# Kernel tuning notes

Hardware: AMD Instinct MI355X
Metric: run time of the kernel (lower is better)

The kernel has to match this reference:

```python
import jax, jax.numpy as jnp
import numpy as np

T, B, F = 512, 256, 256
H1, H2, OUT = 128, 64, 5


def _gru_layer(x, w_ih, w_hh, b_ih, b_hh):
    """PyTorch-convention GRU over time-major x [T, B, F_in] -> [T, B, H].
    Gate order in weights: r, z, n. n = tanh(Wn x + bn_i + r * (Un h + bn_h))."""
    H = w_hh.shape[1]
    # Precompute input projections for all timesteps: [T, B, 3H]
    xp = jnp.einsum('tbf,gf->tbg', x, w_ih) + b_ih

    def step(h, xp_t):
        hp = h @ w_hh.T + b_hh  # [B, 3H]
        xr, xz, xn = jnp.split(xp_t, 3, axis=-1)
        hr, hz, hn = jnp.split(hp, 3, axis=-1)
        r = jax.nn.sigmoid(xr + hr)
        z = jax.nn.sigmoid(xz + hz)
        n = jnp.tanh(xn + r * hn)
        h_new = (1.0 - z) * n + z * h
        return h_new, h_new

    h0 = jnp.zeros((x.shape[1], H), dtype=x.dtype)
    _, ys = jax.lax.scan(step, h0, xp)
    return ys  # [T, B, H]


def setup_inputs() -> dict:
    key = jax.random.key(0)
    ks = jax.random.split(key, 12)
    s1 = 1.0 / np.sqrt(H1)
    s2 = 1.0 / np.sqrt(H2)
    return {
        'x': jax.random.normal(ks[0], (T, B, F), dtype=jnp.float32),
        'w_ih1': jax.random.uniform(ks[1], (3 * H1, F), jnp.float32, -s1, s1),
        'w_hh1': jax.random.uniform(ks[2], (3 * H1, H1), jnp.float32, -s1, s1),
        'b_ih1': jax.random.uniform(ks[3], (3 * H1,), jnp.float32, -s1, s1),
        'b_hh1': jax.random.uniform(ks[4], (3 * H1,), jnp.float32, -s1, s1),
        'w_ih2': jax.random.uniform(ks[5], (3 * H2, H1), jnp.float32, -s2, s2),
        'w_hh2': jax.random.uniform(ks[6], (3 * H2, H2), jnp.float32, -s2, s2),
        'b_ih2': jax.random.uniform(ks[7], (3 * H2,), jnp.float32, -s2, s2),
        'b_hh2': jax.random.uniform(ks[8], (3 * H2,), jnp.float32, -s2, s2),
        'lin_w': jax.random.uniform(ks[9], (OUT, H2), jnp.float32, -s2, s2),
        'lin_b': jax.random.uniform(ks[10], (OUT,), jnp.float32, -s2, s2),
    }


def reference(x, w_ih1, w_hh1, b_ih1, b_hh1, w_ih2, w_hh2, b_ih2, b_hh2, lin_w, lin_b):
    h1 = _gru_layer(x, w_ih1, w_hh1, b_ih1, b_hh1)   # [T, B, 128]
    h2 = _gru_layer(h1, w_ih2, w_hh2, b_ih2, b_hh2)  # [T, B, 64]
    # Faithful to the original: x[:, -1, :] selects the last BATCH element
    # across all timesteps (time-major layout), giving [T, 64].
    last = h2[:, -1, :]
    return last @ lin_w.T + lin_b  # [T, 5]
```

## Files before the change

### kernel.cpp

```cpp
#include <hip/hip_runtime.h>
#include <hip/hip_bf16.h>

#define T_STEPS 512
#define BATCH   256
#define FDIM    256
#define H1      128
#define H2      64
#define OUT_N   5
#define CAT     (H1 + H2)
#define LOG2E   1.4426950408889634f

#if __has_builtin(__builtin_amdgcn_exp2f)
#define EXP2F(x) __builtin_amdgcn_exp2f(x)
#else
#define EXP2F(x) exp2f(x)
#endif
#if __has_builtin(__builtin_amdgcn_rcpf)
#define RCPF(x) __builtin_amdgcn_rcpf(x)
#else
#define RCPF(x) (1.0f / (x))
#endif

template<int CTRL>
__device__ __forceinline__ float dpp_add(float v) {
    int s = __builtin_amdgcn_update_dpp(0, __float_as_int(v), CTRL, 0xF, 0xF, true);
    return v + __int_as_float(s);
}
__device__ __forceinline__ float sig_scaled(float a) {
    return RCPF(1.0f + EXP2F(a));
}
__device__ __forceinline__ float tanh_scaled(float a) {
    return fmaf(-2.0f, RCPF(EXP2F(a) + 1.0f), 1.0f);
}

__global__ __launch_bounds__(256) void xp1_kernel(
    const float* __restrict__ x,
    const float* __restrict__ w_ih1,
    const float* __restrict__ b_ih1,
    const float* __restrict__ b_hh1,
    float* __restrict__ xp)
{
    __shared__ float xrow[FDIM];
    const int t = blockIdx.x;
    const float* xr = x + (size_t)t * BATCH * FDIM + (size_t)(BATCH - 1) * FDIM;
    if (threadIdx.x < FDIM / 4) {
        ((float4*)xrow)[threadIdx.x] = ((const float4*)xr)[threadIdx.x];
    }
    __syncthreads();
    const int q = threadIdx.x >> 2;
    const int s = threadIdx.x & 3;
    #pragma unroll
    for (int pass = 0; pass < 6; ++pass) {
        const int g = pass * 64 + q;
        const float* w = w_ih1 + (size_t)g * FDIM + (s << 2);
        float acc = 0.0f;
        #pragma unroll
        for (int c = 0; c < 16; ++c) {
            float4 wv = *(const float4*)(w + 16 * c);
            const float* xv = xrow + (s << 2) + 16 * c;
            acc = fmaf(wv.x, xv[0], acc);
            acc = fmaf(wv.y, xv[1], acc);
            acc = fmaf(wv.z, xv[2], acc);
            acc = fmaf(wv.w, xv[3], acc);
        }
        acc = dpp_add<0xB1>(acc);
        acc = dpp_add<0x4E>(acc);
        if (s == 0) {
            const bool isN = (g >= 2 * H1);
            const float badd  = isN ? 0.0f : b_hh1[g];
            const float scale = isN ? (2.0f * LOG2E) : (-LOG2E);
            xp[t * (3 * H1) + g] = scale * (acc + b_ih1[g] + badd);
        }
    }
}

__global__ __launch_bounds__(1024) void gru_seq_kernel(
    const float* __restrict__ xp,
    const float* __restrict__ w_hh1, const float* __restrict__ b_hh1,
    const float* __restrict__ w_ih2, const float* __restrict__ b_ih2,
    const float* __restrict__ w_hh2, const float* __restrict__ b_hh2,
    float* __restrict__ h2_all)
{
    const int tid = threadIdx.x;
    __shared__ float cat0[CAT];
    __shared__ float cat1[CAT];
    if (tid < CAT) { cat0[tid] = 0.0f; cat1[tid] = 0.0f; }

    const float sRZ = -LOG2E, sN = 2.0f * LOG2E;

    if (tid < 512) {
        const int j1 = tid >> 2, s1 = tid & 3;
        float w1r[32], w1z[32], w1n[32];
        {
            const float* br = w_hh1 + (size_t)(         j1) * H1;
            const float* bz = w_hh1 + (size_t)(H1     + j1) * H1;
            const float* bn = w_hh1 + (size_t)(2 * H1 + j1) * H1;
            #pragma unroll
            for (int c = 0; c < 8; c++) {
                const int kk = (s1 << 2) + 16 * c;
                float4 vr = *(const float4*)(br + kk);
                float4 vz = *(const float4*)(bz + kk);
                float4 vn = *(const float4*)(bn + kk);
                w1r[4*c+0]=sRZ*vr.x; w1r[4*c+1]=sRZ*vr.y; w1r[4*c+2]=sRZ*vr.z; w1r[4*c+3]=sRZ*vr.w;
                w1z[4*c+0]=sRZ*vz.x; w1z[4*c+1]=sRZ*vz.y; w1z[4*c+2]=sRZ*vz.z; w1z[4*c+3]=sRZ*vz.w;
                w1n[4*c+0]=sN *vn.x; w1n[4*c+1]=sN *vn.y; w1n[4*c+2]=sN *vn.z; w1n[4*c+3]=sN *vn.w;
            }
        }
        const float bh1n_s = sN * b_hh1[2 * H1 + j1];
        const float* xq = xp + j1;
        float cxr = xq[0], cxz = xq[H1], cxn = xq[2 * H1];
        xq += 3 * H1;
        __syncthreads();

        {
            float nr = xq[0], nz = xq[H1], nn = xq[2 * H1]; xq += 3 * H1;
            const float r1 = sig_scaled(cxr);
            const float z1 = sig_scaled(cxz);
            const float n1 = tanh_scaled(fmaf(r1, bh1n_s, cxn));
            if (s1 == 0) cat0[j1] = (1.0f - z1) * n1;
            cxr = nr; cxz = nz; cxn = nn;
            __syncthreads();
        }

        #define L1_STEP(RP, WP, PREF) do {                                              \
            const float* hp = RP + (s1 << 2);                                           \
            float ar = 0.f, az = 0.f, an = 0.f;                                         \
            _Pragma("unroll")                                                           \
            for (int c = 0; c < 8; c++) {                                               \
                float4 h4 = *(const float4*)(hp + 16 * c);                              \
                ar=fmaf(w1r[4*c+0],h4.x,ar); az=fmaf(w1z[4*c+0],h4.x,az); an=fmaf(w1n[4*c+0],h4.x,an); \
                ar=fmaf(w1r[4*c+1],h4.y,ar); az=fmaf(w1z[4*c+1],h4.y,az); an=fmaf(w1n[4*c+1],h4.y,an); \
                ar=fmaf(w1r[4*c+2],h4.z,ar); az=fmaf(w1z[4*c+2],h4.z,az); an=fmaf(w1n[4*c+2],h4.z,an); \
                ar=fmaf(w1r[4*c+3],h4.w,ar); az=fmaf(w1z[4*c+3],h4.w,az); an=fmaf(w1n[4*c+3],h4.w,an); \
            }                                                                           \
            const float h1old = RP[j1];                                                 \
            float nr = 0.f, nz = 0.f, nn = 0.f;                                         \
            if (PREF) { nr = xq[0]; nz = xq[H1]; nn = xq[2 * H1]; xq += 3 * H1; }       \
            ar = dpp_add<0xB1>(ar); ar = dpp_add<0x4E>(ar);                             \
            az = dpp_add<0xB1>(az); az = dpp_add<0x4E>(az);                             \
            an = dpp_add<0xB1>(an); an = dpp_add<0x4E>(an);                             \
            const float r1 = sig_scaled(cxr + ar);                                      \
            const float z1 = sig_scaled(cxz + az);                                      \
            const float n1 = tanh_scaled(fmaf(r1, an + bh1n_s, cxn));                   \
            if (s1 == 0) WP[j1] = fmaf(z1, h1old - n1, n1);                             \
            cxr = nr; cxz = nz; cxn = nn;                                               \
        } while (0)

        #pragma unroll 1
        for (int i = 0; i < 255; i++) {
            L1_STEP(cat0, cat1, true);
            __syncthreads();
            L1_STEP(cat1, cat0, true);
            __syncthreads();
        }
        L1_STEP(cat0, cat1, false);
        __syncthreads();
        __syncthreads();
        #undef L1_STEP
    } else {
        const int t2 = tid - 512;
        const int j2 = t2 >> 3, s2 = t2 & 7;
        float w2r[24], w2z[24], w2n[24];
        {
            const float* ir  = w_ih2 + (size_t)(         j2) * H1;
            const float* iz  = w_ih2 + (size_t)(H2     + j2) * H1;
            const float* inn = w_ih2 + (size_t)(2 * H2 + j2) * H1;
            #pragma unroll
            for (int c = 0; c < 4; c++) {
                const int kk = (s2 << 2) + 32 * c;
                float4 vr = *(const float4*)(ir  + kk);
                float4 vz = *(const float4*)(iz  + kk);
                float4 vn = *(const float4*)(inn + kk);
                w2r[4*c+0]=sRZ*vr.x; w2r[4*c+1]=sRZ*vr.y; w2r[4*c+2]=sRZ*vr.z; w2r[4*c+3]=sRZ*vr.w;
                w2z[4*c+0]=sRZ*vz.x; w2z[4*c+1]=sRZ*vz.y; w2z[4*c+2]=sRZ*vz.z; w2z[4*c+3]=sRZ*vz.w;
                w2n[4*c+0]=sN *vn.x; w2n[4*c+1]=sN *vn.y; w2n[4*c+2]=sN *vn.z; w2n[4*c+3]=sN *vn.w;
            }
            const float* hr = w_hh2 + (size_t)(         j2) * H2;
            const float* hz = w_hh2 + (size_t)(H2     + j2) * H2;
            const float* hn = w_hh2 + (size_t)(2 * H2 + j2) * H2;
            #pragma unroll
            for (int c = 0; c < 2; c++) {
                const int kk = (s2 << 2) + 32 * c;
                const int o = 4 * (c + 4);
                float4 vr = *(const float4*)(hr + kk);
                float4 vz = *(const float4*)(hz + kk);
                float4 vn = *(const float4*)(hn + kk);
                w2r[o+0]=sRZ*vr.x; w2r[o+1]=sRZ*vr.y; w2r[o+2]=sRZ*vr.z; w2r[o+3]=sRZ*vr.w;
                w2z[o+0]=sRZ*vz.x; w2z[o+1]=sRZ*vz.y; w2z[o+2]=sRZ*vz.z; w2z[o+3]=sRZ*vz.w;
                w2n[o+0]=sN *vn.x; w2n[o+1]=sN *vn.y; w2n[o+2]=sN *vn.z; w2n[o+3]=sN *vn.w;
            }
        }
        const float b2r_s  = sRZ * (b_ih2[j2]      + b_hh2[j2]);
        const float b2z_s  = sRZ * (b_ih2[H2 + j2] + b_hh2[H2 + j2]);
        const float b2xn_s = sN  *  b_ih2[2 * H2 + j2];
        const float b2hn_s = sN  *  b_hh2[2 * H2 + j2];
        float* hout = h2_all + j2;
        __syncthreads();
        __syncthreads();

        #define L2_STEP(RP, WP) do {                                                    \
            const float* gp = RP + (s2 << 2);                                           \
            float a2r = 0.f, a2z = 0.f, axn = 0.f, ahn = 0.f;                           \
            _Pragma("unroll")                                                           \
            for (int c = 0; c < 4; c++) {                                               \
                float4 g4 = *(const float4*)(gp + 32 * c);                              \
                a2r=fmaf(w2r[4*c+0],g4.x,a2r); a2z=fmaf(w2z[4*c+0],g4.x,a2z); axn=fmaf(w2n[4*c+0],g4.x,axn); \
                a2r=fmaf(w2r[4*c+1],g4.y,a2r); a2z=fmaf(w2z[4*c+1],g4.y,a2z); axn=fmaf(w2n[4*c+1],g4.y,axn); \
                a2r=fmaf(w2r[4*c+2],g4.z,a2r); a2z=fmaf(w2z[4*c+2],g4.z,a2z); axn=fmaf(w2n[4*c+2],g4.z,axn); \
                a2r=fmaf(w2r[4*c+3],g4.w,a2r); a2z=fmaf(w2z[4*c+3],g4.w,a2z); axn=fmaf(w2n[4*c+3],g4.w,axn); \
            }                                                                           \
            _Pragma("unroll")                                                           \
            for (int c = 4; c < 6; c++) {                                               \
                float4 g4 = *(const float4*)(gp + 32 * c);                              \
                a2r=fmaf(w2r[4*c+0],g4.x,a2r); a2z=fmaf(w2z[4*c+0],g4.x,a2z); ahn=fmaf(w2n[4*c+0],g4.x,ahn); \
                a2r=fmaf(w2r[4*c+1],g4.y,a2r); a2z=fmaf(w2z[4*c+1],g4.y,a2z); ahn=fmaf(w2n[4*c+1],g4.y,ahn); \
                a2r=fmaf(w2r[4*c+2],g4.z,a2r); a2z=fmaf(w2z[4*c+2],g4.z,a2z); ahn=fmaf(w2n[4*c+2],g4.z,ahn); \
                a2r=fmaf(w2r[4*c+3],g4.w,a2r); a2z=fmaf(w2z[4*c+3],g4.w,a2z); ahn=fmaf(w2n[4*c+3],g4.w,ahn); \
            }                                                                           \
            const float h2old = RP[H1 + j2];                                            \
            a2r = dpp_add<0xB1>(a2r); a2r = dpp_add<0x4E>(a2r); a2r = dpp_add<0x141>(a2r); \
            a2z = dpp_add<0xB1>(a2z); a2z = dpp_add<0x4E>(a2z); a2z = dpp_add<0x141>(a2z); \
            axn = dpp_add<0xB1>(axn); axn = dpp_add<0x4E>(axn); axn = dpp_add<0x141>(axn); \
            ahn = dpp_add<0xB1>(ahn); ahn = dpp_add<0x4E>(ahn); ahn = dpp_add<0x141>(ahn); \
            const float r2 = sig_scaled(a2r + b2r_s);                                   \
            const float z2 = sig_scaled(a2z + b2z_s);                                   \
            const float n2 = tanh_scaled(fmaf(r2, ahn + b2hn_s, axn + b2xn_s));         \
            const float h2new = fmaf(z2, h2old - n2, n2);                               \
            if (s2 == 0) { WP[H1 + j2] = h2new; *hout = h2new; }                        \
            hout += H2;                                                                 \
        } while (0)

        #pragma unroll 1
        for (int i = 0; i < 255; i++) {
            L2_STEP(cat0, cat1);
            __syncthreads();
            L2_STEP(cat1, cat0);
            __syncthreads();
        }
        L2_STEP(cat0, cat1);
        __syncthreads();
        L2_STEP(cat1, cat0);
        __syncthreads();
        #undef L2_STEP
    }
}

__global__ __launch_bounds__(256) void head_kernel(
    const float* __restrict__ h2_all,
    const float* __restrict__ lin_w,
    const float* __restrict__ lin_b,
    float* __restrict__ out)
{
    const int t = blockIdx.x * blockDim.x + threadIdx.x;
    if (t >= T_STEPS) return;
    const float* h = h2_all + t * H2;
    #pragma unroll
    for (int o = 0; o < OUT_N; o++) {
        float acc = lin_b[o];
        const float* w = lin_w + o * H2;
        #pragma unroll
        for (int j = 0; j < H2; j += 4) {
            float4 wv = *(const float4*)(w + j);
            float4 hv = *(const float4*)(h + j);
            acc = fmaf(wv.x, hv.x, acc);
            acc = fmaf(wv.y, hv.y, acc);
            acc = fmaf(wv.z, hv.z, acc);
            acc = fmaf(wv.w, hv.w, acc);
        }
        out[t * OUT_N + o] = acc;
    }
}

extern "C" void kernel_launch(void* const* d_in, const int* in_sizes, int n_in,
                              void* d_out, int out_size, void* d_ws, size_t ws_size,
                              hipStream_t stream) {
    const float* x     = (const float*)d_in[0];
    const float* w_ih1 = (const float*)d_in[1];
    const float* w_hh1 = (const float*)d_in[2];
    const float* b_ih1 = (const float*)d_in[3];
    const float* b_hh1 = (const float*)d_in[4];
    const float* w_ih2 = (const float*)d_in[5];
    const float* w_hh2 = (const float*)d_in[6];
    const float* b_ih2 = (const float*)d_in[7];
    const float* b_hh2 = (const float*)d_in[8];
    const float* lin_w = (const float*)d_in[9];
    const float* lin_b = (const float*)d_in[10];
    float* out = (float*)d_out;

    float* xp     = (float*)d_ws;
    float* h2_all = xp + T_STEPS * 3 * H1;

    xp1_kernel<<<T_STEPS, 256, 0, stream>>>(x, w_ih1, b_ih1, b_hh1, xp);
    gru_seq_kernel<<<1, 1024, 0, stream>>>(xp, w_hh1, b_hh1,
                                           w_ih2, b_ih2, w_hh2, b_hh2, h2_all);
    head_kernel<<<(T_STEPS + 255) / 256, 256, 0, stream>>>(h2_all, lin_w, lin_b, out);
}
```

Measured before the change: 542.8 us.

## Regroup layer-1 threads to two rows each, use lighter barriers, keep h in registers

Layer-1 threads now compute two hidden rows over an 8-lane k-split instead of one row over a 4-lane split, and each lane selects its row's result after a three-stage DPP reduction. The previous hidden state for both layers is held in a register rather than reloaded from shared memory. __syncthreads is replaced by a custom barrier that waits only on LDS counters and not on global memory, so global prefetches of xp can stay in flight across steps. The peeled first step is folded into the main loop. The intent is to shorten the serial per-step critical path, at the cost of more FMAs per thread and extra DPP and select work.

Result: no change. 535.9 us (-1.3%).

```diff
diff --git a/kernel.cpp b/kernel.cpp
--- a/kernel.cpp
+++ b/kernel.cpp
@@ -20,6 +20,11 @@
 #else
 #define RCPF(x) (1.0f / (x))
 #endif
+
+#define BAR() do {                                              \
+    asm volatile("s_waitcnt lgkmcnt(0)" ::: "memory");          \
+    __builtin_amdgcn_s_barrier();                               \
+} while (0)
 
 template<int CTRL>
 __device__ __forceinline__ float dpp_add(float v) {
@@ -89,74 +94,97 @@
     const float sRZ = -LOG2E, sN = 2.0f * LOG2E;
 
     if (tid < 512) {
-        const int j1 = tid >> 2, s1 = tid & 3;
-        float w1r[32], w1z[32], w1n[32];
+        const int g  = tid >> 3;
+        const int s  = tid & 7;
+        const int hi = (tid >> 2) & 1;
+        const int r0 = 2 * g;
+
+        float wr0[16], wz0[16], wn0[16], wr1[16], wz1[16], wn1[16];
         {
-            const float* br = w_hh1 + (size_t)(         j1) * H1;
-            const float* bz = w_hh1 + (size_t)(H1     + j1) * H1;
-            const float* bn = w_hh1 + (size_t)(2 * H1 + j1) * H1;
+            const float* br0 = w_hh1 + (size_t)(         r0) * H1;
+            const float* bz0 = w_hh1 + (size_t)(H1     + r0) * H1;
+            const float* bn0 = w_hh1 + (size_t)(2 * H1 + r0) * H1;
             #pragma unroll
-            for (int c = 0; c < 8; c++) {
-                const int kk = (s1 << 2) + 16 * c;
-                float4 vr = *(const float4*)(br + kk);
-                float4 vz = *(const float4*)(bz + kk);
-                float4 vn = *(const float4*)(bn + kk);
-                w1r[4*c+0]=sRZ*vr.x; w1r[4*c+1]=sRZ*vr.y; w1r[4*c+2]=sRZ*vr.z; w1r[4*c+3]=sRZ*vr.w;
-                w1z[4*c+0]=sRZ*vz.x; w1z[4*c+1]=sRZ*vz.y; w1z[4*c+2]=sRZ*vz.z; w1z[4*c+3]=sRZ*vz.w;
-                w1n[4*c+0]=sN *vn.x; w1n[4*c+1]=sN *vn.y; w1n[4*c+2]=sN *vn.z; w1n[4*c+3]=sN *vn.w;
+            for (int c = 0; c < 4; c++) {
+                const int kk = (s << 2) + 32 * c;
+                float4 v0 = *(const float4*)(br0 + kk);
+                float4 v1 = *(const float4*)(bz0 + kk);
+                float4 v2 = *(const float4*)(bn0 + kk);
+                float4 v3 = *(const float4*)(br0 + H1 + kk);
+                float4 v4 = *(const float4*)(bz0 + H1 + kk);
+                float4 v5 = *(const float4*)(bn0 + H1 + kk);
+                wr0[4*c+0]=sRZ*v0.x; wr0[4*c+1]=sRZ*v0.y; wr0[4*c+2]=sRZ*v0.z; wr0[4*c+3]=sRZ*v0.w;
+                wz0[4*c+0]=sRZ*v1.x; wz0[4*c+1]=sRZ*v1.y; wz0[4*c+2]=sRZ*v1.z; wz0[4*c+3]=sRZ*v1.w;
+                wn0[4*c+0]=sN *v2.x; wn0[4*c+1]=sN *v2.y; wn0[4*c+2]=sN *v2.z; wn0[4*c+3]=sN *v2.w;
+                wr1[4*c+0]=sRZ*v3.x; wr1[4*c+1]=sRZ*v3.y; wr1[4*c+2]=sRZ*v3.z; wr1[4*c+3]=sRZ*v3.w;
+                wz1[4*c+0]=sRZ*v4.x; wz1[4*c+1]=sRZ*v4.y; wz1[4*c+2]=sRZ*v4.z; wz1[4*c+3]=sRZ*v4.w;
+                wn1[4*c+0]=sN *v5.x; wn1[4*c+1]=sN *v5.y; wn1[4*c+2]=sN *v5.z; wn1[4*c+3]=sN *v5.w;
             }
         }
-        const float bh1n_s = sN * b_hh1[2 * H1 + j1];
-        const float* xq = xp + j1;
-        float cxr = xq[0], cxz = xq[H1], cxn = xq[2 * H1];
-        xq += 3 * H1;
-        __syncthreads();
-
+        const float bn_a = sN * b_hh1[2 * H1 + r0];
+        const float bn_b = sN * b_hh1[2 * H1 + r0 + 1];
+        const float bh1n_s = hi ? bn_b : bn_a;
+
+        float h1prev = 0.0f;
+        float cxr, cxz, cxn;
         {
-            float nr = xq[0], nz = xq[H1], nn = xq[2 * H1]; xq += 3 * H1;
-            const float r1 = sig_scaled(cxr);
-            const float z1 = sig_scaled(cxz);
-            const float n1 = tanh_scaled(fmaf(r1, bh1n_s, cxn));
-            if (s1 == 0) cat0[j1] = (1.0f - z1) * n1;
-            cxr = nr; cxz = nz; cxn = nn;
-            __syncthreads();
-        }
-
-        #define L1_STEP(RP, WP, PREF) do {                                              \
-            const float* hp = RP + (s1 << 2);                                           \
-            float ar = 0.f, az = 0.f, an = 0.f;                                         \
+            float2 a2 = *(const float2*)(xp + r0);
+            float2 b2 = *(const float2*)(xp + H1 + r0);
+            float2 c2 = *(const float2*)(xp + 2 * H1 + r0);
+            cxr = hi ? a2.y : a2.x; cxz = hi ? b2.y : b2.x; cxn = hi ? c2.y : c2.x;
+        }
+        BAR();
+
+        #define L1_BODY(RP, WP, K) do {                                                 \
+            const float* hp = RP + (s << 2);                                            \
+            float ar0=0.f, az0=0.f, an0=0.f, ar1=0.f, az1=0.f, an1=0.f;                 \
             _Pragma("unroll")                                                           \
-            for (int c = 0; c < 8; c++) {                                               \
-                float4 h4 = *(const float4*)(hp + 16 * c);                              \
-                ar=fmaf(w1r[4*c+0],h4.x,ar); az=fmaf(w1z[4*c+0],h4.x,az); an=fmaf(w1n[4*c+0],h4.x,an); \
-                ar=fmaf(w1r[4*c+1],h4.y,ar); az=fmaf(w1z[4*c+1],h4.y,az); an=fmaf(w1n[4*c+1],h4.y,an); \
-                ar=fmaf(w1r[4*c+2],h4.z,ar); az=fmaf(w1z[4*c+2],h4.z,az); an=fmaf(w1n[4*c+2],h4.z,an); \
-                ar=fmaf(w1r[4*c+3],h4.w,ar); az=fmaf(w1z[4*c+3],h4.w,az); an=fmaf(w1n[4*c+3],h4.w,an); \
+            for (int cc = 0; cc < 4; cc++) {                                            \
+                float4 h4 = *(const float4*)(hp + 32 * cc);                             \
+                ar0=fmaf(wr0[4*cc+0],h4.x,ar0); az0=fmaf(wz0[4*cc+0],h4.x,az0); an0=fmaf(wn0[4*cc+0],h4.x,an0); \
+                ar1=fmaf(wr1[4*cc+0],h4.x,ar1); az1=fmaf(wz1[4*cc+0],h4.x,az1); an1=fmaf(wn1[4*cc+0],h4.x,an1); \
+                ar0=fmaf(wr0[4*cc+1],h4.y,ar0); az0=fmaf(wz0[4*cc+1],h4.y,az0); an0=fmaf(wn0[4*cc+1],h4.y,an0); \
+                ar1=fmaf(wr1[4*cc+1],h4.y,ar1); az1=fmaf(wz1[4*cc+1],h4.y,az1); an1=fmaf(wn1[4*cc+1],h4.y,an1); \
+                ar0=fmaf(wr0[4*cc+2],h4.z,ar0); az0=fmaf(wz0[4*cc+2],h4.z,az0); an0=fmaf(wn0[4*cc+2],h4.z,an0); \
+                ar1=fmaf(wr1[4*cc+2],h4.z,ar1); az1=fmaf(wz1[4*cc+2],h4.z,az1); an1=fmaf(wn1[4*cc+2],h4.z,an1); \
+                ar0=fmaf(wr0[4*cc+3],h4.w,ar0); az0=fmaf(wz0[4*cc+3],h4.w,az0); an0=fmaf(wn0[4*cc+3],h4.w,an0); \
+                ar1=fmaf(wr1[4*cc+3],h4.w,ar1); az1=fmaf(wz1[4*cc+3],h4.w,az1); an1=fmaf(wn1[4*cc+3],h4.w,an1); \
             }                                                                           \
-            const float h1old = RP[j1];                                                 \
-            float nr = 0.f, nz = 0.f, nn = 0.f;                                         \
-            if (PREF) { nr = xq[0]; nz = xq[H1]; nn = xq[2 * H1]; xq += 3 * H1; }       \
-            ar = dpp_add<0xB1>(ar); ar = dpp_add<0x4E>(ar);                             \
-            az = dpp_add<0xB1>(az); az = dpp_add<0x4E>(az);                             \
-            an = dpp_add<0xB1>(an); an = dpp_add<0x4E>(an);                             \
-            const float r1 = sig_scaled(cxr + ar);                                      \
-            const float z1 = sig_scaled(cxz + az);                                      \
-            const float n1 = tanh_scaled(fmaf(r1, an + bh1n_s, cxn));                   \
-            if (s1 == 0) WP[j1] = fmaf(z1, h1old - n1, n1);                             \
-            cxr = nr; cxz = nz; cxn = nn;                                               \
+            float2 a2, b2, c2;                                                          \
+            {                                                                           \
+                const int kn = ((K) < T_STEPS - 1) ? ((K) + 1) : (T_STEPS - 1);         \
+                const float* nx = xp + (size_t)kn * (3 * H1);                           \
+                a2 = *(const float2*)(nx + r0);                                         \
+                b2 = *(const float2*)(nx + H1 + r0);                                    \
+                c2 = *(const float2*)(nx + 2 * H1 + r0);                                \
+            }                                                                           \
+            ar0=dpp_add<0xB1>(ar0); ar0=dpp_add<0x4E>(ar0); ar0=dpp_add<0x141>(ar0);    \
+            az0=dpp_add<0xB1>(az0); az0=dpp_add<0x4E>(az0); az0=dpp_add<0x141>(az0);    \
+            an0=dpp_add<0xB1>(an0); an0=dpp_add<0x4E>(an0); an0=dpp_add<0x141>(an0);    \
+            ar1=dpp_add<0xB1>(ar1); ar1=dpp_add<0x4E>(ar1); ar1=dpp_add<0x141>(ar1);    \
+            az1=dpp_add<0xB1>(az1); az1=dpp_add<0x4E>(az1); az1=dpp_add<0x141>(az1);    \
+            an1=dpp_add<0xB1>(an1); an1=dpp_add<0x4E>(an1); an1=dpp_add<0x141>(an1);    \
+            const float ar = hi ? ar1 : ar0;                                            \
+            const float az = hi ? az1 : az0;                                            \
+            const float an = hi ? an1 : an0;                                            \
+            const float r1g = sig_scaled(cxr + ar);                                     \
+            const float z1g = sig_scaled(cxz + az);                                     \
+            const float n1g = tanh_scaled(fmaf(r1g, an + bh1n_s, cxn));                 \
+            const float h1new = fmaf(z1g, h1prev - n1g, n1g);                           \
+            h1prev = h1new;                                                             \
+            if ((tid & 3) == 0) WP[r0 + hi] = h1new;                                    \
+            cxr = hi ? a2.y : a2.x; cxz = hi ? b2.y : b2.x; cxn = hi ? c2.y : c2.x;     \
         } while (0)
 
         #pragma unroll 1
-        for (int i = 0; i < 255; i++) {
-            L1_STEP(cat0, cat1, true);
-            __syncthreads();
-            L1_STEP(cat1, cat0, true);
-            __syncthreads();
-        }
-        L1_STEP(cat0, cat1, false);
-        __syncthreads();
-        __syncthreads();
-        #undef L1_STEP
+        for (int i = 0; i < 256; i++) {
+            L1_BODY(cat1, cat0, 2 * i);
+            BAR();
+            L1_BODY(cat0, cat1, 2 * i + 1);
+            BAR();
+        }
+        BAR();
+        #undef L1_BODY
     } else {
         const int t2 = tid - 512;
         const int j2 = t2 >> 3, s2 = t2 & 7;
@@ -194,54 +222,51 @@
         const float b2z_s  = sRZ * (b_ih2[H2 + j2] + b_hh2[H2 + j2]);
         const float b2xn_s = sN  *  b_ih2[2 * H2 + j2];
         const float b2hn_s = sN  *  b_hh2[2 * H2 + j2];
+        float h2prev = 0.0f;
         float* hout = h2_all + j2;
-        __syncthreads();
-        __syncthreads();
-
-        #define L2_STEP(RP, WP) do {                                                    \
+        BAR();
+        BAR();
+
+        #define L2_BODY(RP, WP) do {                                                    \
             const float* gp = RP + (s2 << 2);                                           \
             float a2r = 0.f, a2z = 0.f, axn = 0.f, ahn = 0.f;                           \
             _Pragma("unroll")                                                           \
-            for (int c = 0; c < 4; c++) {                                               \
-                float4 g4 = *(const float4*)(gp + 32 * c);                              \
-                a2r=fmaf(w2r[4*c+0],g4.x,a2r); a2z=fmaf(w2z[4*c+0],g4.x,a2z); axn=fmaf(w2n[4*c+0],g4.x,axn); \
-                a2r=fmaf(w2r[4*c+1],g4.y,a2r); a2z=fmaf(w2z[4*c+1],g4.y,a2z); axn=fmaf(w2n[4*c+1],g4.y,axn); \
-                a2r=fmaf(w2r[4*c+2],g4.z,a2r); a2z=fmaf(w2z[4*c+2],g4.z,a2z); axn=fmaf(w2n[4*c+2],g4.z,axn); \
-                a2r=fmaf(w2r[4*c+3],g4.w,a2r); a2z=fmaf(w2z[4*c+3],g4.w,a2z); axn=fmaf(w2n[4*c+3],g4.w,axn); \
+            for (int cc = 0; cc < 4; cc++) {                                            \
+                float4 g4 = *(const float4*)(gp + 32 * cc);                             \
+                a2r=fmaf(w2r[4*cc+0],g4.x,a2r); a2z=fmaf(w2z[4*cc+0],g4.x,a2z); axn=fmaf(w2n[4*cc+0],g4.x,axn); \
+                a2r=fmaf(w2r[4*cc+1],g4.y,a2r); a2z=fmaf(w2z[4*cc+1],g4.y,a2z); axn=fmaf(w2n[4*cc+1],g4.y,axn); \
+                a2r=fmaf(w2r[4*cc+2],g4.z,a2r); a2z=fmaf(w2z[4*cc+2],g4.z,a2z); axn=fmaf(w2n[4*cc+2],g4.z,axn); \
+                a2r=fmaf(w2r[4*cc+3],g4.w,a2r); a2z=fmaf(w2z[4*cc+3],g4.w,a2z); axn=fmaf(w2n[4*cc+3],g4.w,axn); \
             }                                                                           \
             _Pragma("unroll")                                                           \
-            for (int c = 4; c < 6; c++) {                                               \
-                float4 g4 = *(const float4*)(gp + 32 * c);                              \
-                a2r=fmaf(w2r[4*c+0],g4.x,a2r); a2z=fmaf(w2z[4*c+0],g4.x,a2z); ahn=fmaf(w2n[4*c+0],g4.x,ahn); \
-                a2r=fmaf(w2r[4*c+1],g4.y,a2r); a2z=fmaf(w2z[4*c+1],g4.y,a2z); ahn=fmaf(w2n[4*c+1],g4.y,ahn); \
-                a2r=fmaf(w2r[4*c+2],g4.z,a2r); a2z=fmaf(w2z[4*c+2],g4.z,a2z); ahn=fmaf(w2n[4*c+2],g4.z,ahn); \
-                a2r=fmaf(w2r[4*c+3],g4.w,a2r); a2z=fmaf(w2z[4*c+3],g4.w,a2z); ahn=fmaf(w2n[4*c+3],g4.w,ahn); \
+            for (int cc = 4; cc < 6; cc++) {                                            \
+                float4 g4 = *(const float4*)(gp + 32 * cc);                             \
+                a2r=fmaf(w2r[4*cc+0],g4.x,a2r); a2z=fmaf(w2z[4*cc+0],g4.x,a2z); ahn=fmaf(w2n[4*cc+0],g4.x,ahn); \
+                a2r=fmaf(w2r[4*cc+1],g4.y,a2r); a2z=fmaf(w2z[4*cc+1],g4.y,a2z); ahn=fmaf(w2n[4*cc+1],g4.y,ahn); \
+                a2r=fmaf(w2r[4*cc+2],g4.z,a2r); a2z=fmaf(w2z[4*cc+2],g4.z,a2z); ahn=fmaf(w2n[4*cc+2],g4.z,ahn); \
+                a2r=fmaf(w2r[4*cc+3],g4.w,a2r); a2z=fmaf(w2z[4*cc+3],g4.w,a2z); ahn=fmaf(w2n[4*cc+3],g4.w,ahn); \
             }                                                                           \
-            const float h2old = RP[H1 + j2];                                            \
-            a2r = dpp_add<0xB1>(a2r); a2r = dpp_add<0x4E>(a2r); a2r = dpp_add<0x141>(a2r); \
-            a2z = dpp_add<0xB1>(a2z); a2z = dpp_add<0x4E>(a2z); a2z = dpp_add<0x141>(a2z); \
-            axn = dpp_add<0xB1>(axn); axn = dpp_add<0x4E>(axn); axn = dpp_add<0x141>(axn); \
-            ahn = dpp_add<0xB1>(ahn); ahn = dpp_add<0x4E>(ahn); ahn = dpp_add<0x141>(ahn); \
+            a2r=dpp_add<0xB1>(a2r); a2r=dpp_add<0x4E>(a2r); a2r=dpp_add<0x141>(a2r);    \
+            a2z=dpp_add<0xB1>(a2z); a2z=dpp_add<0x4E>(a2z); a2z=dpp_add<0x141>(a2z);    \
+            axn=dpp_add<0xB1>(axn); axn=dpp_add<0x4E>(axn); axn=dpp_add<0x141>(axn);    \
+            ahn=dpp_add<0xB1>(ahn); ahn=dpp_add<0x4E>(ahn); ahn=dpp_add<0x141>(ahn);    \
             const float r2 = sig_scaled(a2r + b2r_s);                                   \
             const float z2 = sig_scaled(a2z + b2z_s);                                   \
             const float n2 = tanh_scaled(fmaf(r2, ahn + b2hn_s, axn + b2xn_s));         \
-            const float h2new = fmaf(z2, h2old - n2, n2);                               \
+            const float h2new = fmaf(z2, h2prev - n2, n2);                              \
+            h2prev = h2new;                                                             \
             if (s2 == 0) { WP[H1 + j2] = h2new; *hout = h2new; }                        \
             hout += H2;                                                                 \
         } while (0)
 
         #pragma unroll 1
-        for (int i = 0; i < 255; i++) {
-            L2_STEP(cat0, cat1);
-            __syncthreads();
-            L2_STEP(cat1, cat0);
-            __syncthreads();
-        }
-        L2_STEP(cat0, cat1);
-        __syncthreads();
-        L2_STEP(cat1, cat0);
-        __syncthreads();
-        #undef L2_STEP
+        for (int i = 0; i < 256; i++) {
+            L2_BODY(cat0, cat1);
+            BAR();
+            L2_BODY(cat1, cat0);
+            BAR();
+        }
+        #undef L2_BODY
     }
 }
 
```
